# Optimization experiments

Measured on AMD Instinct MI355X. Metric: run time of the kernel, lower is better.

Reference implementation:

```python
import jax, jax.numpy as jnp
import numpy as np

IN_FEATURES = 4096
OUT_FEATURES = 11008
GROUP_SIZE = 128
NUM_GROUPS = IN_FEATURES // GROUP_SIZE  # 32


def setup_inputs() -> dict:
    key = jax.random.key(0)
    k1, k2, k3, k4 = jax.random.split(key, 4)
    x = jax.random.normal(k1, (8192, IN_FEATURES), dtype=jnp.float32)
    # packed 4-bit weights: one uint8 byte holds two 4-bit values
    qweight = jax.random.randint(k2, (IN_FEATURES * OUT_FEATURES // 2,), 0, 256, dtype=jnp.int32)
    qzeros = jax.random.randint(k3, (OUT_FEATURES, NUM_GROUPS), 0, 16, dtype=jnp.int32)
    scales = jax.random.uniform(k4, (OUT_FEATURES, NUM_GROUPS), dtype=jnp.float32) * 0.01
    return {"x": x, "qweight": qweight, "qzeros": qzeros, "scales": scales}


def _dequantize(qweight, qzeros, scales):
    # unpack: low nibble first, then high nibble (matches stack([low, high], dim=1).view(-1))
    b = qweight.astype(jnp.int32)
    low = b & 15
    high = (b >> 4) & 15
    w = jnp.stack([low, high], axis=1).reshape(-1)  # [in*out]
    w = w[: OUT_FEATURES * IN_FEATURES].reshape(OUT_FEATURES, IN_FEATURES).astype(jnp.float32)
    # per-group dequant: (w - zero) * scale, groups along in_features
    w = w.reshape(OUT_FEATURES, NUM_GROUPS, GROUP_SIZE)
    w = (w - qzeros[:, :, None].astype(jnp.float32)) * scales[:, :, None]
    return w.reshape(OUT_FEATURES, IN_FEATURES)


def reference(x, qweight, qzeros, scales) -> jnp.ndarray:
    weight = _dequantize(qweight, qzeros, scales).astype(x.dtype)  # [out, in]
    # F.linear(x, W) = x @ W.T
    return jnp.einsum("bi,oi->bo", x, weight)
```

## Files before the change

### kernel.cpp

```cpp
#include <hip/hip_runtime.h>
#include <hip/hip_bf16.h>


#define IN_F   4096
#define OUT_F  11008
#define M_DIM  8192
#define NGROUP 32

typedef __bf16 bf16x8 __attribute__((ext_vector_type(8)));
typedef float  f32x4  __attribute__((ext_vector_type(4)));
typedef unsigned short u16;
typedef u16 u16x8v __attribute__((ext_vector_type(8)));

__device__ __forceinline__ u16 f2bf(float f) {
  union { float f; unsigned u; } v; v.f = f;
  unsigned u = v.u;
  return (u16)((u + 0x7fffu + ((u >> 16) & 1u)) >> 16);
}

__device__ __forceinline__ void gload_lds16(const void* gsrc, void* ldst) {
  __builtin_amdgcn_global_load_lds(
      (const __attribute__((address_space(1))) void*)gsrc,
      (__attribute__((address_space(3))) void*)ldst, 16, 0, 0);
}

__global__ __launch_bounds__(256) void dequant_w(const int* __restrict__ qw,
                                                 const int* __restrict__ qz,
                                                 const float* __restrict__ sc,
                                                 u16* __restrict__ W) {
  const int total = (IN_F / 2) * OUT_F / 4;
  int stride = gridDim.x * blockDim.x;
  for (int idx = blockIdx.x * blockDim.x + threadIdx.x; idx < total; idx += stride) {
    int j = idx << 2;
    int o = j >> 11;
    int g = (j >> 6) & 31;
    float z = (float)qz[(o << 5) + g];
    float s = sc[(o << 5) + g];
    int4 q = ((const int4*)qw)[idx];
    int qs0 = q.x, qs1 = q.y, qs2 = q.z, qs3 = q.w;
    u16x8v w;
    w[0] = f2bf(((float)(qs0 & 15) - z) * s);
    w[1] = f2bf(((float)((qs0 >> 4) & 15) - z) * s);
    w[2] = f2bf(((float)(qs1 & 15) - z) * s);
    w[3] = f2bf(((float)((qs1 >> 4) & 15) - z) * s);
    w[4] = f2bf(((float)(qs2 & 15) - z) * s);
    w[5] = f2bf(((float)((qs2 >> 4) & 15) - z) * s);
    w[6] = f2bf(((float)(qs3 & 15) - z) * s);
    w[7] = f2bf(((float)((qs3 >> 4) & 15) - z) * s);
    ((u16x8v*)W)[idx] = w;
  }
}

__global__ __launch_bounds__(256) void cvt_x(const float* __restrict__ x,
                                             u16* __restrict__ Xb) {
  const int total = M_DIM * IN_F / 8;
  int stride = gridDim.x * blockDim.x;
  for (int idx = blockIdx.x * blockDim.x + threadIdx.x; idx < total; idx += stride) {
    float4 a = ((const float4*)x)[idx * 2];
    float4 b = ((const float4*)x)[idx * 2 + 1];
    u16x8v v;
    v[0] = f2bf(a.x); v[1] = f2bf(a.y); v[2] = f2bf(a.z); v[3] = f2bf(a.w);
    v[4] = f2bf(b.x); v[5] = f2bf(b.y); v[6] = f2bf(b.z); v[7] = f2bf(b.w);
    ((u16x8v*)Xb)[idx] = v;
  }
}


#define BAR       __builtin_amdgcn_s_barrier()
#define SCHED0    __builtin_amdgcn_sched_barrier(0)
#define LGKM0     asm volatile("s_waitcnt lgkmcnt(0)" ::: "memory")
#define VMCNT4    asm volatile("s_waitcnt vmcnt(4)" ::: "memory")
#define VMCNT6    asm volatile("s_waitcnt vmcnt(6)" ::: "memory")
#define PRIO(p)   __builtin_amdgcn_s_setprio(p)

__global__ __launch_bounds__(512, 2) void gemm256(const u16* __restrict__ A,
                                                  const u16* __restrict__ B,
                                                  float* __restrict__ C) {
  constexpr int K = IN_F, N = OUT_F;
  constexpr int NT = K / 64;
  __shared__ __align__(16) u16 sA[2][256 * 64];
  __shared__ __align__(16) u16 sB[2][256 * 64];

  const int NTN = OUT_F / 256;
  const int NWG = (M_DIM / 256) * NTN;
  int bid = blockIdx.x;
  int wg  = (bid & 7) * (NWG / 8) + (bid >> 3);
  int tm = wg / NTN, tn = wg - tm * NTN;
  int m0 = tm * 256, n0 = tn * 256;

  int tid  = threadIdx.x;
  int lane = tid & 63;
  int wave = tid >> 6;
  int wr = wave >> 2, wc = wave & 3;

  int rstage = tid >> 3;
  int gslot  = ((tid & 7) ^ (rstage & 7)) << 3;
  int ldsoff = rstage * 64 + ((tid & 7) << 3);
  const u16* Ag = A + (size_t)(m0 + rstage) * K + gslot;
  const u16* Bg = B + (size_t)(n0 + rstage) * K + gslot;

#define STAGE_A(cb, h, kt) do {                                   \
    const u16* _g = Ag + (size_t)(h) * 128 * K + (kt) * 64;       \
    u16* _l = sA[cb] + (h) * 128 * 64 + ldsoff;                   \
    gload_lds16(_g, _l);                                          \
    gload_lds16(_g + (size_t)64 * K, _l + 64 * 64);               \
  } while (0)

#define STAGE_B(cb, h, kt) do {                                   \
    const u16* _g = Bg + (size_t)(h) * 128 * K + (kt) * 64;       \
    u16* _l = sB[cb] + (h) * 128 * 64 + ldsoff;                   \
    gload_lds16(_g, _l);                                          \
    gload_lds16(_g + (size_t)64 * K, _l + 64 * 64);               \
  } while (0)

  int q8  = lane >> 4;
  int sl0 = ((q8 ^ (lane & 7)) << 3);
  int sl1 = (((q8 | 4) ^ (lane & 7)) << 3);
  int abase = (wr * 64 + (lane & 15)) * 64;
  int bbase = (wc * 32 + (lane & 15)) * 64;

  bf16x8 a_[8], b0_[4], b1_[4];
  f32x4 acc[8][4] = {};

#define LDA(cb, mh) do {                                          \
    const u16* _p = sA[cb] + abase + (mh) * 8192;                 \
    a_[0] = *(const bf16x8*)(_p + sl0);                           \
    a_[1] = *(const bf16x8*)(_p + sl1);                           \
    a_[2] = *(const bf16x8*)(_p + 1024 + sl0);                    \
    a_[3] = *(const bf16x8*)(_p + 1024 + sl1);                    \
    a_[4] = *(const bf16x8*)(_p + 2048 + sl0);                    \
    a_[5] = *(const bf16x8*)(_p + 2048 + sl1);                    \
    a_[6] = *(const bf16x8*)(_p + 3072 + sl0);                    \
    a_[7] = *(const bf16x8*)(_p + 3072 + sl1);                    \
  } while (0)

#define LDB(cb, nh, dst) do {                                     \
    const u16* _p = sB[cb] + bbase + (nh) * 8192;                 \
    dst[0] = *(const bf16x8*)(_p + sl0);                          \
    dst[1] = *(const bf16x8*)(_p + sl1);                          \
    dst[2] = *(const bf16x8*)(_p + 1024 + sl0);                   \
    dst[3] = *(const bf16x8*)(_p + 1024 + sl1);                   \
  } while (0)

#define QUAD(mh, nh, bq) do {                                                  \
    _Pragma("unroll") for (int mf = 0; mf < 4; mf++)                           \
      _Pragma("unroll") for (int nf = 0; nf < 2; nf++) {                       \
        acc[(mh)*4+mf][(nh)*2+nf] = __builtin_amdgcn_mfma_f32_16x16x32_bf16(   \
            a_[mf*2+0], bq[nf*2+0], acc[(mh)*4+mf][(nh)*2+nf], 0, 0, 0);       \
        acc[(mh)*4+mf][(nh)*2+nf] = __builtin_amdgcn_mfma_f32_16x16x32_bf16(   \
            a_[mf*2+1], bq[nf*2+1], acc[(mh)*4+mf][(nh)*2+nf], 0, 0, 0);       \
      }                                                                        \
  } while (0)

#define QUAD_ROLLA(mh, nh, bq, rp) do {                                        \
    _Pragma("unroll") for (int mf = 0; mf < 4; mf++) {                         \
      _Pragma("unroll") for (int nf = 0; nf < 2; nf++) {                       \
        acc[(mh)*4+mf][(nh)*2+nf] = __builtin_amdgcn_mfma_f32_16x16x32_bf16(   \
            a_[mf*2+0], bq[nf*2+0], acc[(mh)*4+mf][(nh)*2+nf], 0, 0, 0);       \
        acc[(mh)*4+mf][(nh)*2+nf] = __builtin_amdgcn_mfma_f32_16x16x32_bf16(   \
            a_[mf*2+1], bq[nf*2+1], acc[(mh)*4+mf][(nh)*2+nf], 0, 0, 0);       \
      }                                                                        \
      a_[mf*2+0] = *(const bf16x8*)((rp) + mf * 1024 + sl0);                   \
      a_[mf*2+1] = *(const bf16x8*)((rp) + mf * 1024 + sl1);                   \
    }                                                                          \
  } while (0)

#define TILE(c, u) do {                                           \
    int _k1 = ((u) + 1) & (NT - 1), _k2 = ((u) + 2) & (NT - 1);   \
                                                          \
    STAGE_A((c) ^ 1, 1, _k1);                                     \
    BAR; LGKM0; PRIO(1);                                          \
    LDB(c, 1, b1_);                                               \
    QUAD(0, 0, b0_);                                              \
    PRIO(0); BAR;                                                 \
                                                          \
    STAGE_A(c, 0, _k2);                                           \
    BAR; LGKM0; PRIO(1);                                          \
    QUAD_ROLLA(0, 1, b1_, sA[c] + abase + 8192);                  \
    PRIO(0); BAR;                                                 \
                                                          \
    STAGE_B(c, 0, _k2);                                           \
    BAR; LGKM0; PRIO(1);                                          \
    QUAD(1, 0, b0_);                                              \
    PRIO(0); VMCNT4; BAR;                                         \
                                                          \
    STAGE_B(c, 1, _k2);                                           \
    BAR; LGKM0; PRIO(1);                                          \
    LDB((c) ^ 1, 0, b0_);                                         \
    QUAD_ROLLA(1, 1, b1_, sA[(c) ^ 1] + abase);                   \
    PRIO(0); BAR;                                                 \
  } while (0)

  STAGE_A(0, 0, 0); STAGE_A(0, 1, 0);
  STAGE_B(0, 0, 0); STAGE_B(0, 1, 0);
  STAGE_A(1, 0, 1); STAGE_B(1, 0, 1); STAGE_B(1, 1, 1);
  VMCNT6; BAR;
  SCHED0;
  asm volatile("" ::: "memory");
  LDA(0, 0);
  LDB(0, 0, b0_);

#pragma unroll 1
  for (int u = 0; u < NT; u += 2) {
    TILE(0, u);
    TILE(1, u + 1);
  }

  float* Cp = C + (size_t)(m0 + wr * 64 + ((lane >> 4) << 2)) * N
                + n0 + wc * 32 + (lane & 15);
#pragma unroll
  for (int m = 0; m < 8; m++) {
    int roff = (m >> 2) * 128 + (m & 3) * 16;
#pragma unroll
    for (int n = 0; n < 4; n++) {
      int coff = (n >> 1) * 128 + (n & 1) * 16;
#pragma unroll
      for (int j = 0; j < 4; j++)
        Cp[(size_t)(roff + j) * N + coff] = acc[m][n][j];
    }
  }
}

__global__ __launch_bounds__(256) void naive_gemm(const float* __restrict__ x,
                                                  const int* __restrict__ qw,
                                                  const int* __restrict__ qz,
                                                  const float* __restrict__ sc,
                                                  float* __restrict__ out) {
  __shared__ float xs[IN_F];
  int m = blockIdx.y;
  int n = blockIdx.x * 256 + threadIdx.x;
  for (int i = threadIdx.x; i < IN_F; i += 256) xs[i] = x[(size_t)m * IN_F + i];
  __syncthreads();
  float acc = 0.f;
  const int* qrow = qw + (size_t)n * (IN_F / 2);
  for (int g = 0; g < NGROUP; g++) {
    float z = (float)qz[n * NGROUP + g];
    float s = sc[n * NGROUP + g];
    for (int t = 0; t < 64; t++) {
      int q = qrow[g * 64 + t];
      acc += xs[g * 128 + 2 * t] * ((float)(q & 15) - z) * s;
      acc += xs[g * 128 + 2 * t + 1] * ((float)((q >> 4) & 15) - z) * s;
    }
  }
  out[(size_t)m * OUT_F + n] = acc;
}

extern "C" void kernel_launch(void* const* d_in, const int* in_sizes, int n_in,
                              void* d_out, int out_size, void* d_ws, size_t ws_size,
                              hipStream_t stream) {
  const float* x  = (const float*)d_in[0];
  const int*   qw = (const int*)d_in[1];
  const int*   qz = (const int*)d_in[2];
  const float* sc = (const float*)d_in[3];
  float* out = (float*)d_out;

  const size_t WBYTES = (size_t)OUT_F * IN_F * 2;
  const size_t XBYTES = (size_t)M_DIM * IN_F * 2;

  if (ws_size >= WBYTES + XBYTES) {
    u16* Wb = (u16*)d_ws;
    u16* Xb = (u16*)((char*)d_ws + WBYTES);
    dequant_w<<<2048, 256, 0, stream>>>(qw, qz, sc, Wb);
    cvt_x<<<2048, 256, 0, stream>>>(x, Xb);
    gemm256<<<(M_DIM / 256) * (OUT_F / 256), 512, 0, stream>>>(Xb, Wb, out);
  } else {
    naive_gemm<<<dim3(OUT_F / 256, M_DIM), 256, 0, stream>>>(x, qw, qz, sc, out);
  }
}
```

Before: 723.4 us.

## Restructure GEMM main loop into two phases with fewer barriers

The per-tile schedule of the bf16 MFMA GEMM goes from four barrier-separated phases to two. Each phase issues two global-to-LDS stage loads, then runs two MFMA quads. The B fragment load for the next half-tile moves to the end of the tile, and the prologue staging is reordered to match. The aim is to halve barrier and waitcnt synchronisation and give loads more MFMA work to hide behind. The cost is longer windows in flight and a risk of LDS read/write hazards if the buffer reuse ordering is wrong.

```diff
diff --git a/kernel.cpp b/kernel.cpp
--- a/kernel.cpp
+++ b/kernel.cpp
@@ -69,8 +69,8 @@
 #define BAR       __builtin_amdgcn_s_barrier()
 #define SCHED0    __builtin_amdgcn_sched_barrier(0)
 #define LGKM0     asm volatile("s_waitcnt lgkmcnt(0)" ::: "memory")
+#define VMCNT0    asm volatile("s_waitcnt vmcnt(0)" ::: "memory")
 #define VMCNT4    asm volatile("s_waitcnt vmcnt(4)" ::: "memory")
-#define VMCNT6    asm volatile("s_waitcnt vmcnt(6)" ::: "memory")
 #define PRIO(p)   __builtin_amdgcn_s_setprio(p)
 
 __global__ __launch_bounds__(512, 2) void gemm256(const u16* __restrict__ A,
@@ -165,45 +165,41 @@
     }                                                                          \
   } while (0)
 
-#define TILE(c, u) do {                                           \
+#define TILE2(c, u) do {                                          \
     int _k1 = ((u) + 1) & (NT - 1), _k2 = ((u) + 2) & (NT - 1);   \
-                                                          \
+                      \
     STAGE_A((c) ^ 1, 1, _k1);                                     \
-    BAR; LGKM0; PRIO(1);                                          \
-    LDB(c, 1, b1_);                                               \
+    STAGE_A(c, 0, _k2);                                           \
+    PRIO(1);                                                      \
     QUAD(0, 0, b0_);                                              \
-    PRIO(0); BAR;                                                 \
-                                                          \
-    STAGE_A(c, 0, _k2);                                           \
-    BAR; LGKM0; PRIO(1);                                          \
     QUAD_ROLLA(0, 1, b1_, sA[c] + abase + 8192);                  \
-    PRIO(0); BAR;                                                 \
-                                                          \
+    PRIO(0); VMCNT4; LGKM0; BAR;                                  \
+                      \
     STAGE_B(c, 0, _k2);                                           \
-    BAR; LGKM0; PRIO(1);                                          \
+    STAGE_B(c, 1, _k2);                                           \
+    PRIO(1);                                                      \
     QUAD(1, 0, b0_);                                              \
-    PRIO(0); VMCNT4; BAR;                                         \
-                                                          \
-    STAGE_B(c, 1, _k2);                                           \
-    BAR; LGKM0; PRIO(1);                                          \
     LDB((c) ^ 1, 0, b0_);                                         \
     QUAD_ROLLA(1, 1, b1_, sA[(c) ^ 1] + abase);                   \
-    PRIO(0); BAR;                                                 \
+    LDB((c) ^ 1, 1, b1_);                                         \
+    PRIO(0); VMCNT4; LGKM0; BAR;                                  \
   } while (0)
 
   STAGE_A(0, 0, 0); STAGE_A(0, 1, 0);
   STAGE_B(0, 0, 0); STAGE_B(0, 1, 0);
-  STAGE_A(1, 0, 1); STAGE_B(1, 0, 1); STAGE_B(1, 1, 1);
-  VMCNT6; BAR;
+  STAGE_A(1, 0, 1);
+  VMCNT0; BAR;
   SCHED0;
   asm volatile("" ::: "memory");
   LDA(0, 0);
   LDB(0, 0, b0_);
+  LDB(0, 1, b1_);
+  STAGE_B(1, 0, 1); STAGE_B(1, 1, 1);
 
 #pragma unroll 1
   for (int u = 0; u < NT; u += 2) {
-    TILE(0, u);
-    TILE(1, u + 1);
+    TILE2(0, u);
+    TILE2(1, u + 1);
   }
 
   float* Cp = C + (size_t)(m0 + wr * 64 + ((lane >> 4) << 2)) * N
```

Measured after the change: 709.5 us. Within noise of the previous version (-1.9%).
